# Kernel optimization log

Measured on AMD Instinct MI355X. Metric: run time of the kernel, lower is better.

Reference implementation:

```python
import jax, jax.numpy as jnp
import numpy as np

T, D, N, K, H, F = 2048, 4096, 32, 8, 128, 14336
THETA = 500000.0
EPS = 1e-5


def setup_inputs() -> dict:
    key = jax.random.key(0)
    ks = jax.random.split(key, 10)
    s = 0.02  # weight init scale
    return {
        "x": jax.random.normal(ks[0], (T, D), jnp.float32),
        "positions": jnp.arange(T, dtype=jnp.int32),
        "ln1_scale": jnp.ones((D,), jnp.float32),
        "w_q": jax.random.normal(ks[1], (D, N, H), jnp.float32) * s,
        "w_k": jax.random.normal(ks[2], (D, K, H), jnp.float32) * s,
        "w_v": jax.random.normal(ks[3], (D, K, H), jnp.float32) * s,
        "w_o": jax.random.normal(ks[4], (N, H, D), jnp.float32) * s,
        "ln2_scale": jnp.ones((D,), jnp.float32),
        "w_gate": jax.random.normal(ks[5], (D, F), jnp.float32) * s,
        "w_up": jax.random.normal(ks[6], (D, F), jnp.float32) * s,
        "w_down": jax.random.normal(ks[7], (F, D), jnp.float32) * s,
    }


def _rms_norm(x, scale):
    var = jnp.mean(jnp.square(x), axis=-1, keepdims=True)
    return x * jax.lax.rsqrt(var + EPS) * scale


def _apply_rope(x, pos):
    # x: [T, heads, H]; Llama rotate-half RoPE
    half = H // 2
    inv_freq = 1.0 / (THETA ** (jnp.arange(half, dtype=jnp.float32) / half))
    ang = pos.astype(jnp.float32)[:, None] * inv_freq[None, :]      # [T, half]
    cos = jnp.cos(ang)[:, None, :]
    sin = jnp.sin(ang)[:, None, :]
    x1, x2 = x[..., :half], x[..., half:]
    return jnp.concatenate([x1 * cos - x2 * sin, x2 * cos + x1 * sin], axis=-1)


def reference(x, positions, ln1_scale, w_q, w_k, w_v, w_o, ln2_scale, w_gate, w_up, w_down):
    # --- input RMSNorm ---
    h = _rms_norm(x, ln1_scale)
    # --- QKV projections + RoPE ---
    q = _apply_rope(jnp.einsum('td,dnh->tnh', h, w_q), positions)   # [T,N,H]
    k = _apply_rope(jnp.einsum('td,dkh->tkh', h, w_k), positions)   # [T,K,H]
    v = jnp.einsum('td,dkh->tkh', h, w_v)                            # [T,K,H]
    # --- GQA causal attention (prefill) ---
    G = N // K
    qg = q.reshape(T, K, G, H)
    scale = 1.0 / jnp.sqrt(jnp.float32(H))
    scores = jnp.einsum('tkgh,skh->kgts', qg, k) * scale             # [K,G,T,T]
    causal = positions[:, None] >= positions[None, :]                # [T,T]
    scores = jnp.where(causal[None, None], scores, jnp.finfo(scores.dtype).min)
    probs = jax.nn.softmax(scores, axis=-1)
    attn = jnp.einsum('kgts,skh->tkgh', probs, v).reshape(T, N, H)
    attn_out = jnp.einsum('tnh,nhd->td', attn, w_o)
    # --- residual ---
    residual = attn_out + x
    # --- post-attn RMSNorm + SwiGLU MLP ---
    h2 = _rms_norm(residual, ln2_scale)
    gate = jax.nn.silu(h2 @ w_gate)
    up = h2 @ w_up
    out = (gate * up) @ w_down
    return residual + out
```

## Files before the change

### kernel.cpp

```cpp
#include <hip/hip_runtime.h>

typedef __attribute__((ext_vector_type(8))) short bf16x8;
typedef __attribute__((ext_vector_type(4))) float f32x4;

constexpr int T = 2048;
constexpr int D = 4096;
constexpr int NQ = 32;
constexpr int NKV = 8;
constexpr int H = 128;
constexpr int F = 14336;
constexpr int NQKV = (NQ + 2 * NKV) * H;
constexpr int VOFF = (NQ + NKV) * H;

__device__ inline unsigned short f2bf(float f) {
  unsigned u = __float_as_uint(f);
  return (unsigned short)((u + 0x7FFFu + ((u >> 16) & 1u)) >> 16);
}

__device__ inline void gload_lds16(const void* g, void* l) {
  __builtin_amdgcn_global_load_lds((const __attribute__((address_space(1))) void*)g,
                                   (__attribute__((address_space(3))) void*)l, 16, 0, 0);
}

#define MFMA16(a, b, c) __builtin_amdgcn_mfma_f32_16x16x32_bf16(a, b, c, 0, 0, 0)

template <int MODE>
__global__ __launch_bounds__(256) void transpose_bf16(const float* __restrict__ in,
                                                      unsigned short* __restrict__ out,
                                                      int K, int N) {
  __shared__ float tile[64 * 65];
  const int kb = blockIdx.x * 64;
  const int nb = blockIdx.y * 64;
  const int tid = threadIdx.x;
  const int r = tid >> 2;
  const int c4 = tid & 3;
#pragma unroll
  for (int i = 0; i < 4; ++i) {
    float4 v = *(const float4*)(in + (size_t)(kb + r) * N + nb + c4 * 16 + i * 4);
    *(float4*)&tile[r * 65 + c4 * 16 + i * 4] = v;
  }
  __syncthreads();
  const int n = tid >> 2;
  const int kq = tid & 3;
  int nsrc = nb + n;
  int prow = (MODE == 0) ? nsrc : ((nsrc >> 4) * 32 + (nsrc & 15) + (MODE == 2 ? 16 : 0));
#pragma unroll
  for (int half = 0; half < 2; ++half) {
    ushort4 o0, o1;
    int k0 = kq * 16 + half * 8;
    o0.x = f2bf(tile[(k0 + 0) * 65 + n]);
    o0.y = f2bf(tile[(k0 + 1) * 65 + n]);
    o0.z = f2bf(tile[(k0 + 2) * 65 + n]);
    o0.w = f2bf(tile[(k0 + 3) * 65 + n]);
    o1.x = f2bf(tile[(k0 + 4) * 65 + n]);
    o1.y = f2bf(tile[(k0 + 5) * 65 + n]);
    o1.z = f2bf(tile[(k0 + 6) * 65 + n]);
    o1.w = f2bf(tile[(k0 + 7) * 65 + n]);
    unsigned short* op = out + (size_t)prow * K + kb + k0;
    *(ushort4*)(op + 0) = o0;
    *(ushort4*)(op + 4) = o1;
  }
}

__global__ __launch_bounds__(256) void rmsnorm_kernel(
    const float* __restrict__ in, const float* __restrict__ scale,
    unsigned short* __restrict__ out) {
  int row = blockIdx.x;
  const float4* xr = (const float4*)(in + (size_t)row * D);
  const float4* sr = (const float4*)scale;
  float4 vals[4];
  float ss = 0.f;
#pragma unroll
  for (int i = 0; i < 4; ++i) {
    float4 v = xr[threadIdx.x + i * 256];
    vals[i] = v;
    ss += v.x * v.x + v.y * v.y + v.z * v.z + v.w * v.w;
  }
#pragma unroll
  for (int off = 32; off; off >>= 1) ss += __shfl_xor(ss, off, 64);
  __shared__ float wsum[4];
  if ((threadIdx.x & 63) == 0) wsum[threadIdx.x >> 6] = ss;
  __syncthreads();
  float r = rsqrtf((wsum[0] + wsum[1] + wsum[2] + wsum[3]) * (1.f / D) + 1e-5f);
#pragma unroll
  for (int i = 0; i < 4; ++i) {
    int vi = threadIdx.x + i * 256;
    float4 v = vals[i];
    float4 s = sr[vi];
    ushort4 o;
    o.x = f2bf(v.x * r * s.x);
    o.y = f2bf(v.y * r * s.y);
    o.z = f2bf(v.z * r * s.z);
    o.w = f2bf(v.w * r * s.w);
    *(ushort4*)(out + (size_t)row * D + (size_t)vi * 4) = o;
  }
}

__global__ __launch_bounds__(256) void rmsnorm_add3(
    const float* __restrict__ a, const float* __restrict__ b,
    const float* __restrict__ c, const float* __restrict__ scale,
    float* __restrict__ residOut, unsigned short* __restrict__ out) {
  int row = blockIdx.x;
  const float4* ar = (const float4*)(a + (size_t)row * D);
  const float4* br = (const float4*)(b + (size_t)row * D);
  const float4* cr = (const float4*)(c + (size_t)row * D);
  const float4* sr = (const float4*)scale;
  float4* rr = (float4*)(residOut + (size_t)row * D);
  float4 vals[4];
  float ss = 0.f;
#pragma unroll
  for (int i = 0; i < 4; ++i) {
    int vi = threadIdx.x + i * 256;
    float4 va = ar[vi], vb = br[vi], vc = cr[vi];
    float4 v;
    v.x = va.x + vb.x + vc.x;
    v.y = va.y + vb.y + vc.y;
    v.z = va.z + vb.z + vc.z;
    v.w = va.w + vb.w + vc.w;
    vals[i] = v;
    ss += v.x * v.x + v.y * v.y + v.z * v.z + v.w * v.w;
  }
#pragma unroll
  for (int off = 32; off; off >>= 1) ss += __shfl_xor(ss, off, 64);
  __shared__ float wsum[4];
  if ((threadIdx.x & 63) == 0) wsum[threadIdx.x >> 6] = ss;
  __syncthreads();
  float r = rsqrtf((wsum[0] + wsum[1] + wsum[2] + wsum[3]) * (1.f / D) + 1e-5f);
#pragma unroll
  for (int i = 0; i < 4; ++i) {
    int vi = threadIdx.x + i * 256;
    float4 v = vals[i];
    rr[vi] = v;
    float4 s = sr[vi];
    ushort4 o;
    o.x = f2bf(v.x * r * s.x);
    o.y = f2bf(v.y * r * s.y);
    o.z = f2bf(v.z * r * s.z);
    o.w = f2bf(v.w * r * s.w);
    *(ushort4*)(out + (size_t)row * D + (size_t)vi * 4) = o;
  }
}

__global__ __launch_bounds__(256) void add3_kernel(const float* __restrict__ a,
                                                   const float* __restrict__ b,
                                                   const float* __restrict__ c,
                                                   float* __restrict__ o) {
  int i = blockIdx.x * 256 + threadIdx.x;
  float4 va = ((const float4*)a)[i];
  float4 vb = ((const float4*)b)[i];
  float4 vc = ((const float4*)c)[i];
  float4 vo;
  vo.x = va.x + vb.x + vc.x;
  vo.y = va.y + vb.y + vc.y;
  vo.z = va.z + vb.z + vc.z;
  vo.w = va.w + vb.w + vc.w;
  ((float4*)o)[i] = vo;
}

__global__ __launch_bounds__(256) void rope_table(const int* __restrict__ pos,
                                                  float* __restrict__ ctab,
                                                  float* __restrict__ stab) {
  int idx = blockIdx.x * 256 + threadIdx.x;
  int t = idx >> 6, i = idx & 63;
  float inv = exp2f(-(float)i * (log2f(500000.0f) / 64.0f));
  float ang = (float)pos[t] * inv;
  ctab[idx] = cosf(ang);
  stab[idx] = sinf(ang);
}

__global__ __launch_bounds__(256) void rope_bf16(const float* __restrict__ x,
                                                 const float* __restrict__ ctab,
                                                 const float* __restrict__ stab,
                                                 unsigned short* __restrict__ out,
                                                 int nheads, int row_stride, float scale) {
  int idx = blockIdx.x * 256 + threadIdx.x;
  int i = idx & 63;
  int tn = idx >> 6;
  int t = tn / nheads;
  int n = tn - t * nheads;
  float c = ctab[t * 64 + i], s = stab[t * 64 + i];
  const float* p = x + (size_t)t * row_stride + n * H;
  float x1 = p[i], x2 = p[i + 64];
  unsigned short* o = out + (size_t)tn * H;
  o[i] = f2bf((x1 * c - x2 * s) * scale);
  o[i + 64] = f2bf((x2 * c + x1 * s) * scale);
}

template <int EP>
__global__ __launch_bounds__(512, 1) void gemm256(
    const unsigned short* __restrict__ A, const unsigned short* __restrict__ Bt,
    float* __restrict__ outF, float* __restrict__ outF2,
    unsigned short* __restrict__ outB, int Kd, int Nd, int Klen) {
  __shared__ unsigned short lds[65536];
  const int tid = threadIdx.x, lane = tid & 63, wv = tid >> 6;
  const int wm = wv >> 2, wn = wv & 3;
  const int rl = lane & 15, g = lane >> 4;
  const int kz = blockIdx.z;
  int raw = blockIdx.x + blockIdx.y * gridDim.x;
  int cpx = (gridDim.x * gridDim.y) >> 3;
  int sid = (raw & 7) * cpx + (raw >> 3);
  int brow = sid % gridDim.x;
  int bcol = sid / gridDim.x;
  const int m0 = brow * 256, n0 = bcol * 256;

  const int l8 = lane >> 3;
  const int scol = ((lane & 7) ^ l8) * 8;
  const int xr = (rl & 7) << 4;
  const int pc0 = (g * 16) ^ xr;
  const int pc1 = (64 + g * 16) ^ xr;

  const char* ldsc = (const char*)lds;
  const unsigned short* gA = A + (size_t)(m0 + wv * 8 + l8) * Kd + kz * Klen + scol;
  const unsigned short* gB = Bt + (size_t)(n0 + wv * 8 + l8) * Kd + kz * Klen + scol;

  f32x4 acc[8][4];
#pragma unroll
  for (int i = 0; i < 8; ++i)
#pragma unroll
    for (int j = 0; j < 4; ++j) acc[i][j] = (f32x4){0.f, 0.f, 0.f, 0.f};

  const int NT = Klen >> 6;

#define STAGE_AL(kt, l)                                                      \
  gload_lds16(gA + (size_t)(kt) * 64 + (size_t)(l) * 64 * Kd,                \
              (void*)&lds[((kt) & 1) * 32768 + (l) * 4096 + wv * 512]);
#define STAGE_BL(kt, l)                                                      \
  gload_lds16(gB + (size_t)(kt) * 64 + (size_t)(l) * 64 * Kd,                \
              (void*)&lds[((kt) & 1) * 32768 + 16384 + (l) * 4096 + wv * 512]);
#define SBAR()                        \
  __builtin_amdgcn_sched_barrier(0);  \
  __builtin_amdgcn_s_barrier();

  STAGE_AL(0, 0); STAGE_AL(0, 1); STAGE_AL(0, 2); STAGE_AL(0, 3);
  STAGE_BL(0, 0); STAGE_BL(0, 1); STAGE_BL(0, 2); STAGE_BL(0, 3);
  STAGE_AL(1, 0); STAGE_AL(1, 1); STAGE_AL(1, 2); STAGE_AL(1, 3);
  STAGE_BL(1, 0); STAGE_BL(1, 1); STAGE_BL(1, 2); STAGE_BL(1, 3);
  asm volatile("s_waitcnt vmcnt(8)" ::: "memory");
  SBAR();

  const int bhalf = (wn >> 1) * 16384;
  const int brl = (wn & 1) * 64;

  for (int kt = 0; kt < NT; ++kt) {
    const int b = kt & 1;
    const char* aB = ldsc + b * 65536 + wm * 16384;
    const char* bB = ldsc + b * 65536 + 32768 + bhalf;
    const bool pre = (kt + 2 < NT);
    bf16x8 aR[8][2], bR[4][2];
#pragma unroll
    for (int mf = 0; mf < 8; ++mf) {
      aR[mf][0] = *(const bf16x8*)(aB + (mf * 16 + rl) * 128 + pc0);
      aR[mf][1] = *(const bf16x8*)(aB + (mf * 16 + rl) * 128 + pc1);
    }
#pragma unroll
    for (int nf = 0; nf < 4; ++nf) {
      bR[nf][0] = *(const bf16x8*)(bB + (brl + nf * 16 + rl) * 128 + pc0);
      bR[nf][1] = *(const bf16x8*)(bB + (brl + nf * 16 + rl) * 128 + pc1);
    }
    SBAR();
    if (pre) {
      STAGE_AL(kt + 2, 0); STAGE_AL(kt + 2, 1);
      STAGE_AL(kt + 2, 2); STAGE_AL(kt + 2, 3);
      STAGE_BL(kt + 2, 0); STAGE_BL(kt + 2, 1);
      STAGE_BL(kt + 2, 2); STAGE_BL(kt + 2, 3);
    }
    __builtin_amdgcn_s_setprio(1);
#pragma unroll
    for (int mf = 0; mf < 8; ++mf)
#pragma unroll
      for (int nf = 0; nf < 4; ++nf) {
        acc[mf][nf] = MFMA16(aR[mf][0], bR[nf][0], acc[mf][nf]);
        acc[mf][nf] = MFMA16(aR[mf][1], bR[nf][1], acc[mf][nf]);
      }
    __builtin_amdgcn_s_setprio(0);
    if (pre) {
      asm volatile("s_waitcnt vmcnt(8)" ::: "memory");
    } else if (kt + 1 < NT) {
      asm volatile("s_waitcnt vmcnt(0)" ::: "memory");
    }
    SBAR();
  }

  const int g4 = g * 4;
  if constexpr (EP == 5) {
    const int acolBase = ((n0 + wn * 64) >> 1) + rl;
#pragma unroll
    for (int mf = 0; mf < 8; ++mf)
#pragma unroll
      for (int p = 0; p < 2; ++p) {
        int acol = acolBase + p * 16;
#pragma unroll
        for (int jj = 0; jj < 4; ++jj) {
          int row = m0 + wm * 128 + mf * 16 + g4 + jj;
          float gg = acc[mf][2 * p][jj];
          float uu = acc[mf][2 * p + 1][jj];
          outB[(size_t)row * F + acol] = f2bf(gg / (1.f + __expf(-gg)) * uu);
        }
      }
  } else if constexpr (EP == 4) {
    if (n0 >= VOFF) {
#pragma unroll
      for (int mf = 0; mf < 8; ++mf)
#pragma unroll
        for (int q = 0; q < 4; ++q) {
          int col = n0 + wn * 64 + q * 16 + rl;
          int row0 = m0 + wm * 128 + mf * 16 + g4;
          ushort4 o;
          o.x = f2bf(acc[mf][q][0]);
          o.y = f2bf(acc[mf][q][1]);
          o.z = f2bf(acc[mf][q][2]);
          o.w = f2bf(acc[mf][q][3]);
          *(ushort4*)&outB[(size_t)(col - VOFF) * T + row0] = o;
        }
    } else {
#pragma unroll
      for (int mf = 0; mf < 8; ++mf)
#pragma unroll
        for (int q = 0; q < 4; ++q) {
          int col = n0 + wn * 64 + q * 16 + rl;
#pragma unroll
          for (int jj = 0; jj < 4; ++jj) {
            int row = m0 + wm * 128 + mf * 16 + g4 + jj;
            outF[(size_t)row * Nd + col] = acc[mf][q][jj];
          }
        }
    }
  } else {
    float* dst = kz ? outF2 : outF;
#pragma unroll
    for (int mf = 0; mf < 8; ++mf)
#pragma unroll
      for (int q = 0; q < 4; ++q) {
        int col = n0 + wn * 64 + q * 16 + rl;
#pragma unroll
        for (int jj = 0; jj < 4; ++jj) {
          int row = m0 + wm * 128 + mf * 16 + g4 + jj;
          dst[(size_t)row * Nd + col] = acc[mf][q][jj];
        }
      }
  }
#undef STAGE_AL
#undef STAGE_BL
#undef SBAR
}

constexpr int KLD = 136;
constexpr int VLD = 72;
constexpr int PLD = 72;

__global__ __launch_bounds__(512) void flash_attn(
    const unsigned short* __restrict__ qbf, const unsigned short* __restrict__ kbf,
    const unsigned short* __restrict__ vtbf, unsigned short* __restrict__ out) {
  __shared__ unsigned short K_lds[64 * KLD];
  __shared__ unsigned short Vt_lds[H * VLD];
  __shared__ unsigned short P_lds[8 * 16 * PLD];

  const int tid = threadIdx.x;
  const int lane = tid & 63;
  const int wv = tid >> 6;
  const int qb = blockIdx.x;
  const int kvh = blockIdx.y;
  const int qh = wv & 3, rh = wv >> 2;
  const int n = kvh * 4 + qh;
  const int g = lane >> 4;
  const int rl = lane & 15;
  const int qrow = qb * 32 + rh * 16;

  bf16x8 qfrag[4];
  {
    const unsigned short* qp = qbf + ((size_t)(qrow + rl) * NQ + n) * H + g * 8;
#pragma unroll
    for (int ks = 0; ks < 4; ++ks) qfrag[ks] = *(const bf16x8*)(qp + ks * 32);
  }

  f32x4 oacc[8];
#pragma unroll
  for (int ob = 0; ob < 8; ++ob) oacc[ob] = (f32x4){0.f, 0.f, 0.f, 0.f};
  float mrun[4] = {-1e30f, -1e30f, -1e30f, -1e30f};
  float lrun[4] = {0.f, 0.f, 0.f, 0.f};

  const int krow = tid >> 3, kseg = (tid & 7) * 16;
  const int vh = tid >> 2, vseg = (tid & 3) * 16;

  const int ktmax = (qb * 32 + 31) >> 6;
  bf16x8 krA, krB, vrA, vrB;
  {
    const unsigned short* kp = kbf + ((size_t)krow * NKV + kvh) * H + kseg;
    krA = *(const bf16x8*)kp;
    krB = *(const bf16x8*)(kp + 8);
    const unsigned short* vp = vtbf + (size_t)(kvh * H + vh) * T + vseg;
    vrA = *(const bf16x8*)vp;
    vrB = *(const bf16x8*)(vp + 8);
  }
  for (int kt = 0; kt <= ktmax; ++kt) {
    const int kbase = kt * 64;
    __syncthreads();
    *(bf16x8*)&K_lds[krow * KLD + kseg] = krA;
    *(bf16x8*)&K_lds[krow * KLD + kseg + 8] = krB;
    *(bf16x8*)&Vt_lds[vh * VLD + vseg] = vrA;
    *(bf16x8*)&Vt_lds[vh * VLD + vseg + 8] = vrB;
    if (kt < ktmax) {
      const unsigned short* kp =
          kbf + ((size_t)(kbase + 64 + krow) * NKV + kvh) * H + kseg;
      krA = *(const bf16x8*)kp;
      krB = *(const bf16x8*)(kp + 8);
      const unsigned short* vp =
          vtbf + (size_t)(kvh * H + vh) * T + kbase + 64 + vseg;
      vrA = *(const bf16x8*)vp;
      vrB = *(const bf16x8*)(vp + 8);
    }
    __syncthreads();

    f32x4 sacc[4];
#pragma unroll
    for (int cb = 0; cb < 4; ++cb) sacc[cb] = (f32x4){0.f, 0.f, 0.f, 0.f};
#pragma unroll
    for (int cb = 0; cb < 4; ++cb)
#pragma unroll
      for (int ks = 0; ks < 4; ++ks) {
        bf16x8 kf = *(const bf16x8*)&K_lds[(cb * 16 + rl) * KLD + ks * 32 + g * 8];
        sacc[cb] = MFMA16(qfrag[ks], kf, sacc[cb]);
      }

    if (kt == ktmax) {
#pragma unroll
      for (int cb = 0; cb < 4; ++cb) {
        int kv_abs = kbase + cb * 16 + rl;
#pragma unroll
        for (int r = 0; r < 4; ++r) {
          if (kv_abs > qrow + g * 4 + r) sacc[cb][r] = -1e30f;
        }
      }
    }

    float mx[4], sm[4], corr[4];
#pragma unroll
    for (int r = 0; r < 4; ++r) {
      float m0 = fmaxf(fmaxf(sacc[0][r], sacc[1][r]), fmaxf(sacc[2][r], sacc[3][r]));
#pragma unroll
      for (int off = 1; off < 16; off <<= 1) m0 = fmaxf(m0, __shfl_xor(m0, off, 64));
      float nm = fmaxf(mrun[r], m0);
      corr[r] = __expf(mrun[r] - nm);
      mrun[r] = nm;
      mx[r] = nm;
    }
#pragma unroll
    for (int cb = 0; cb < 4; ++cb)
#pragma unroll
      for (int r = 0; r < 4; ++r) sacc[cb][r] = __expf(sacc[cb][r] - mx[r]);
#pragma unroll
    for (int r = 0; r < 4; ++r) {
      float s0 = sacc[0][r] + sacc[1][r] + sacc[2][r] + sacc[3][r];
#pragma unroll
      for (int off = 1; off < 16; off <<= 1) s0 += __shfl_xor(s0, off, 64);
      sm[r] = s0;
      lrun[r] = lrun[r] * corr[r] + sm[r];
    }
#pragma unroll
    for (int ob = 0; ob < 8; ++ob)
#pragma unroll
      for (int r = 0; r < 4; ++r) oacc[ob][r] *= corr[r];

#pragma unroll
    for (int cb = 0; cb < 4; ++cb)
#pragma unroll
      for (int r = 0; r < 4; ++r)
        P_lds[(wv * 16 + g * 4 + r) * PLD + cb * 16 + rl] = f2bf(sacc[cb][r]);

    bf16x8 pa[2];
#pragma unroll
    for (int ks = 0; ks < 2; ++ks)
      pa[ks] = *(const bf16x8*)&P_lds[(wv * 16 + rl) * PLD + ks * 32 + g * 8];

#pragma unroll
    for (int ob = 0; ob < 8; ++ob)
#pragma unroll
      for (int ks = 0; ks < 2; ++ks) {
        bf16x8 vf = *(const bf16x8*)&Vt_lds[(ob * 16 + rl) * VLD + ks * 32 + g * 8];
        oacc[ob] = MFMA16(pa[ks], vf, oacc[ob]);
      }
  }

  float inv[4];
#pragma unroll
  for (int r = 0; r < 4; ++r) inv[r] = 1.f / lrun[r];
#pragma unroll
  for (int ob = 0; ob < 8; ++ob)
#pragma unroll
    for (int r = 0; r < 4; ++r) {
      int t = qrow + g * 4 + r;
      out[((size_t)t * NQ + n) * H + ob * 16 + rl] = f2bf(oacc[ob][r] * inv[r]);
    }
}

extern "C" void kernel_launch(void* const* d_in, const int* in_sizes, int n_in,
                              void* d_out, int out_size, void* d_ws, size_t ws_size,
                              hipStream_t stream) {
  (void)in_sizes; (void)n_in; (void)out_size; (void)ws_size;
  const float* x = (const float*)d_in[0];
  const int* positions = (const int*)d_in[1];
  const float* ln1 = (const float*)d_in[2];
  const float* w_q = (const float*)d_in[3];
  const float* w_k = (const float*)d_in[4];
  const float* w_v = (const float*)d_in[5];
  const float* w_o = (const float*)d_in[6];
  const float* ln2 = (const float*)d_in[7];
  const float* w_gate = (const float*)d_in[8];
  const float* w_up = (const float*)d_in[9];
  const float* w_down = (const float*)d_in[10];
  float* out = (float*)d_out;

  char* ws = (char*)d_ws;
  size_t off = 0;
  auto alloc = [&](size_t bytes) {
    char* p = ws + off;
    off += (bytes + 255) & ~(size_t)255;
    return p;
  };
  unsigned short* h_bf = (unsigned short*)alloc((size_t)T * D * 2);
  unsigned short* h2_bf = (unsigned short*)alloc((size_t)T * D * 2);
  unsigned short* attn_bf = (unsigned short*)alloc((size_t)T * NQ * H * 2);
  unsigned short* act_bf = (unsigned short*)alloc((size_t)T * F * 2);
  float* qkvf = (float*)alloc((size_t)T * NQKV * 4);
  float* resid = (float*)alloc((size_t)T * D * 4);
  float* ctab = (float*)alloc((size_t)T * 64 * 4);
  float* stab = (float*)alloc((size_t)T * 64 * 4);
  unsigned short* qbf = (unsigned short*)alloc((size_t)T * NQ * H * 2);
  unsigned short* kbf = (unsigned short*)alloc((size_t)T * NKV * H * 2);
  unsigned short* vtbf = (unsigned short*)alloc((size_t)NKV * H * T * 2);
  unsigned short* wqkvt = (unsigned short*)alloc((size_t)NQKV * D * 2);
  unsigned short* wot = (unsigned short*)alloc((size_t)D * NQ * H * 2);
  unsigned short* wgut = (unsigned short*)alloc((size_t)2 * F * D * 2);
  unsigned short* wdt = (unsigned short*)alloc((size_t)D * F * 2);
  float* part0 = qkvf;
  float* part1 = (float*)wqkvt;

  transpose_bf16<0><<<dim3(D / 64, (NQ * H) / 64), 256, 0, stream>>>(w_q, wqkvt, D, NQ * H);
  transpose_bf16<0><<<dim3(D / 64, (NKV * H) / 64), 256, 0, stream>>>(
      w_k, wqkvt + (size_t)NQ * H * D, D, NKV * H);
  transpose_bf16<0><<<dim3(D / 64, (NKV * H) / 64), 256, 0, stream>>>(
      w_v, wqkvt + (size_t)VOFF * D, D, NKV * H);
  transpose_bf16<0><<<dim3((NQ * H) / 64, D / 64), 256, 0, stream>>>(w_o, wot, NQ * H, D);
  transpose_bf16<1><<<dim3(D / 64, F / 64), 256, 0, stream>>>(w_gate, wgut, D, F);
  transpose_bf16<2><<<dim3(D / 64, F / 64), 256, 0, stream>>>(w_up, wgut, D, F);
  transpose_bf16<0><<<dim3(F / 64, D / 64), 256, 0, stream>>>(w_down, wdt, F, D);

  rmsnorm_kernel<<<T, 256, 0, stream>>>(x, ln1, h_bf);
  rope_table<<<(T * 64) / 256, 256, 0, stream>>>(positions, ctab, stab);
  gemm256<4><<<dim3(T / 256, NQKV / 256, 1), 512, 0, stream>>>(
      h_bf, wqkvt, qkvf, nullptr, vtbf, D, NQKV, D);
  rope_bf16<<<(T * NQ * 64) / 256, 256, 0, stream>>>(qkvf, ctab, stab, qbf, NQ, NQKV,
                                                     0.08838834764831845f);
  rope_bf16<<<(T * NKV * 64) / 256, 256, 0, stream>>>(qkvf + NQ * H, ctab, stab, kbf,
                                                      NKV, NQKV, 1.0f);
  flash_attn<<<dim3(T / 32, NKV), 512, 0, stream>>>(qbf, kbf, vtbf, attn_bf);
  gemm256<0><<<dim3(T / 256, D / 256, 2), 512, 0, stream>>>(
      attn_bf, wot, part0, part1, nullptr, NQ * H, D, NQ * H / 2);
  rmsnorm_add3<<<T, 256, 0, stream>>>(part0, part1, x, ln2, resid, h2_bf);
  gemm256<5><<<dim3(T / 256, (2 * F) / 256), 512, 0, stream>>>(
      h2_bf, wgut, nullptr, nullptr, act_bf, D, 2 * F, D);
  gemm256<0><<<dim3(T / 256, D / 256, 2), 512, 0, stream>>>(
      act_bf, wdt, part0, part1, nullptr, F, D, F / 2);
  add3_kernel<<<(T * D / 4) / 256, 256, 0, stream>>>(part0, part1, resid, out);
}
```

Before: 1.331 ms.

## Split GEMM k-tile into quadrant phases, interleave LDS reads and prefetch; bf16 QK output

Restructures the 256x256 GEMM main loop into four MFMA quadrant phases, with LDS fragment reads and global-to-LDS prefetches spread between them. The low B fragments for the next tile are carried across iterations in registers. The goal is to overlap LDS reads and memory issue with MFMA work instead of loading every fragment up front. The launch bound changes to request two blocks per CU, which limits register use and could cause spills given the 128 accumulator floats. Separately, the QKV GEMM now writes Q and K as bf16 instead of fp32, and the RoPE kernel reads that bf16 input, halving that intermediate traffic at the cost of rounding before RoPE.

```diff
diff --git a/kernel.cpp b/kernel.cpp
--- a/kernel.cpp
+++ b/kernel.cpp
@@ -15,6 +15,10 @@
 __device__ inline unsigned short f2bf(float f) {
   unsigned u = __float_as_uint(f);
   return (unsigned short)((u + 0x7FFFu + ((u >> 16) & 1u)) >> 16);
+}
+
+__device__ inline float bf2f(unsigned short u) {
+  return __uint_as_float((unsigned)u << 16);
 }
 
 __device__ inline void gload_lds16(const void* g, void* l) {
@@ -168,7 +172,7 @@
   stab[idx] = sinf(ang);
 }
 
-__global__ __launch_bounds__(256) void rope_bf16(const float* __restrict__ x,
+__global__ __launch_bounds__(256) void rope_bf16(const unsigned short* __restrict__ x,
                                                  const float* __restrict__ ctab,
                                                  const float* __restrict__ stab,
                                                  unsigned short* __restrict__ out,
@@ -179,15 +183,15 @@
   int t = tn / nheads;
   int n = tn - t * nheads;
   float c = ctab[t * 64 + i], s = stab[t * 64 + i];
-  const float* p = x + (size_t)t * row_stride + n * H;
-  float x1 = p[i], x2 = p[i + 64];
+  const unsigned short* p = x + (size_t)t * row_stride + n * H;
+  float x1 = bf2f(p[i]), x2 = bf2f(p[i + 64]);
   unsigned short* o = out + (size_t)tn * H;
   o[i] = f2bf((x1 * c - x2 * s) * scale);
   o[i + 64] = f2bf((x2 * c + x1 * s) * scale);
 }
 
 template <int EP>
-__global__ __launch_bounds__(512, 1) void gemm256(
+__global__ __launch_bounds__(512, 2) void gemm256(
     const unsigned short* __restrict__ A, const unsigned short* __restrict__ Bt,
     float* __restrict__ outF, float* __restrict__ outF2,
     unsigned short* __restrict__ outB, int Kd, int Nd, int Klen) {
@@ -221,64 +225,113 @@
 
   const int NT = Klen >> 6;
 
-#define STAGE_AL(kt, l)                                                      \
+#define STAGE_AL(kt, bb, l)                                                  \
   gload_lds16(gA + (size_t)(kt) * 64 + (size_t)(l) * 64 * Kd,                \
-              (void*)&lds[((kt) & 1) * 32768 + (l) * 4096 + wv * 512]);
-#define STAGE_BL(kt, l)                                                      \
+              (void*)&lds[(bb) * 32768 + (l) * 4096 + wv * 512]);
+#define STAGE_BL(kt, bb, l)                                                  \
   gload_lds16(gB + (size_t)(kt) * 64 + (size_t)(l) * 64 * Kd,                \
-              (void*)&lds[((kt) & 1) * 32768 + 16384 + (l) * 4096 + wv * 512]);
+              (void*)&lds[(bb) * 32768 + 16384 + (l) * 4096 + wv * 512]);
 #define SBAR()                        \
   __builtin_amdgcn_sched_barrier(0);  \
   __builtin_amdgcn_s_barrier();
 
-  STAGE_AL(0, 0); STAGE_AL(0, 1); STAGE_AL(0, 2); STAGE_AL(0, 3);
-  STAGE_BL(0, 0); STAGE_BL(0, 1); STAGE_BL(0, 2); STAGE_BL(0, 3);
-  STAGE_AL(1, 0); STAGE_AL(1, 1); STAGE_AL(1, 2); STAGE_AL(1, 3);
-  STAGE_BL(1, 0); STAGE_BL(1, 1); STAGE_BL(1, 2); STAGE_BL(1, 3);
+  STAGE_AL(0, 0, 0); STAGE_AL(0, 0, 1); STAGE_AL(0, 0, 2); STAGE_AL(0, 0, 3);
+  STAGE_BL(0, 0, 0); STAGE_BL(0, 0, 1); STAGE_BL(0, 0, 2); STAGE_BL(0, 0, 3);
+  STAGE_AL(1, 1, 0); STAGE_AL(1, 1, 1); STAGE_AL(1, 1, 2); STAGE_AL(1, 1, 3);
+  STAGE_BL(1, 1, 0); STAGE_BL(1, 1, 1); STAGE_BL(1, 1, 2); STAGE_BL(1, 1, 3);
   asm volatile("s_waitcnt vmcnt(8)" ::: "memory");
   SBAR();
 
   const int bhalf = (wn >> 1) * 16384;
   const int brl = (wn & 1) * 64;
 
-  for (int kt = 0; kt < NT; ++kt) {
-    const int b = kt & 1;
-    const char* aB = ldsc + b * 65536 + wm * 16384;
-    const char* bB = ldsc + b * 65536 + 32768 + bhalf;
-    const bool pre = (kt + 2 < NT);
-    bf16x8 aR[8][2], bR[4][2];
-#pragma unroll
-    for (int mf = 0; mf < 8; ++mf) {
-      aR[mf][0] = *(const bf16x8*)(aB + (mf * 16 + rl) * 128 + pc0);
-      aR[mf][1] = *(const bf16x8*)(aB + (mf * 16 + rl) * 128 + pc1);
+  bf16x8 bLoC[2][2];
+  {
+    const char* bB0 = ldsc + 32768 + bhalf;
+#pragma unroll
+    for (int nf = 0; nf < 2; ++nf) {
+      bLoC[nf][0] = *(const bf16x8*)(bB0 + (brl + nf * 16 + rl) * 128 + pc0);
+      bLoC[nf][1] = *(const bf16x8*)(bB0 + (brl + nf * 16 + rl) * 128 + pc1);
     }
-#pragma unroll
-    for (int nf = 0; nf < 4; ++nf) {
-      bR[nf][0] = *(const bf16x8*)(bB + (brl + nf * 16 + rl) * 128 + pc0);
-      bR[nf][1] = *(const bf16x8*)(bB + (brl + nf * 16 + rl) * 128 + pc1);
-    }
-    SBAR();
-    if (pre) {
-      STAGE_AL(kt + 2, 0); STAGE_AL(kt + 2, 1);
-      STAGE_AL(kt + 2, 2); STAGE_AL(kt + 2, 3);
-      STAGE_BL(kt + 2, 0); STAGE_BL(kt + 2, 1);
-      STAGE_BL(kt + 2, 2); STAGE_BL(kt + 2, 3);
-    }
-    __builtin_amdgcn_s_setprio(1);
-#pragma unroll
-    for (int mf = 0; mf < 8; ++mf)
-#pragma unroll
-      for (int nf = 0; nf < 4; ++nf) {
-        acc[mf][nf] = MFMA16(aR[mf][0], bR[nf][0], acc[mf][nf]);
-        acc[mf][nf] = MFMA16(aR[mf][1], bR[nf][1], acc[mf][nf]);
-      }
-    __builtin_amdgcn_s_setprio(0);
-    if (pre) {
-      asm volatile("s_waitcnt vmcnt(8)" ::: "memory");
-    } else if (kt + 1 < NT) {
-      asm volatile("s_waitcnt vmcnt(0)" ::: "memory");
-    }
-    SBAR();
+  }
+
+#define KTILE(kt, bb)                                                          \
+  {                                                                            \
+    const char* aB = ldsc + (bb) * 65536 + wm * 16384;                         \
+    const char* bB = ldsc + (bb) * 65536 + 32768 + bhalf;                      \
+    const char* bBn = ldsc + (1 - (bb)) * 65536 + 32768 + bhalf;               \
+    const bool pre = ((kt) + 2 < NT);                                          \
+    bf16x8 aLo[4][2], aHi[4][2], bHi[2][2], bLoN[2][2];                        \
+    _Pragma("unroll") for (int mf = 0; mf < 4; ++mf) {                         \
+      aLo[mf][0] = *(const bf16x8*)(aB + (mf * 16 + rl) * 128 + pc0);          \
+      aLo[mf][1] = *(const bf16x8*)(aB + (mf * 16 + rl) * 128 + pc1);          \
+    }                                                                          \
+    SBAR();                                                                    \
+    __builtin_amdgcn_s_setprio(1);                                             \
+    _Pragma("unroll") for (int mf = 0; mf < 4; ++mf)                           \
+        _Pragma("unroll") for (int nf = 0; nf < 2; ++nf) {                     \
+      acc[mf][nf] = MFMA16(aLo[mf][0], bLoC[nf][0], acc[mf][nf]);              \
+      acc[mf][nf] = MFMA16(aLo[mf][1], bLoC[nf][1], acc[mf][nf]);              \
+    }                                                                          \
+    __builtin_amdgcn_s_setprio(0);                                             \
+    _Pragma("unroll") for (int nf = 0; nf < 2; ++nf) {                         \
+      bHi[nf][0] = *(const bf16x8*)(bB + (brl + (nf + 2) * 16 + rl) * 128 + pc0); \
+      bHi[nf][1] = *(const bf16x8*)(bB + (brl + (nf + 2) * 16 + rl) * 128 + pc1); \
+    }                                                                          \
+    if (pre) { STAGE_AL((kt) + 2, bb, 0); STAGE_AL((kt) + 2, bb, 2); }         \
+    SBAR();                                                                    \
+    __builtin_amdgcn_s_setprio(1);                                             \
+    _Pragma("unroll") for (int mf = 0; mf < 4; ++mf)                           \
+        _Pragma("unroll") for (int nf = 0; nf < 2; ++nf) {                     \
+      acc[mf][nf + 2] = MFMA16(aLo[mf][0], bHi[nf][0], acc[mf][nf + 2]);       \
+      acc[mf][nf + 2] = MFMA16(aLo[mf][1], bHi[nf][1], acc[mf][nf + 2]);       \
+    }                                                                          \
+    __builtin_amdgcn_s_setprio(0);                                             \
+    _Pragma("unroll") for (int mf = 0; mf < 4; ++mf) {                         \
+      aHi[mf][0] = *(const bf16x8*)(aB + ((mf + 4) * 16 + rl) * 128 + pc0);    \
+      aHi[mf][1] = *(const bf16x8*)(aB + ((mf + 4) * 16 + rl) * 128 + pc1);    \
+    }                                                                          \
+    if (pre) {                                                                 \
+      STAGE_BL((kt) + 2, bb, 0); STAGE_BL((kt) + 2, bb, 1);                    \
+      STAGE_BL((kt) + 2, bb, 2); STAGE_BL((kt) + 2, bb, 3);                    \
+      asm volatile("s_waitcnt vmcnt(6)" ::: "memory");                         \
+    } else {                                                                   \
+      asm volatile("s_waitcnt vmcnt(0)" ::: "memory");                         \
+    }                                                                          \
+    SBAR();                                                                    \
+    __builtin_amdgcn_s_setprio(1);                                             \
+    _Pragma("unroll") for (int mf = 0; mf < 4; ++mf)                           \
+        _Pragma("unroll") for (int nf = 0; nf < 2; ++nf) {                     \
+      acc[mf + 4][nf + 2] = MFMA16(aHi[mf][0], bHi[nf][0], acc[mf + 4][nf + 2]); \
+      acc[mf + 4][nf + 2] = MFMA16(aHi[mf][1], bHi[nf][1], acc[mf + 4][nf + 2]); \
+    }                                                                          \
+    __builtin_amdgcn_s_setprio(0);                                             \
+    if (pre) { STAGE_AL((kt) + 2, bb, 1); STAGE_AL((kt) + 2, bb, 3); }         \
+    if ((kt) + 1 < NT) {                                                       \
+      _Pragma("unroll") for (int nf = 0; nf < 2; ++nf) {                       \
+        bLoN[nf][0] = *(const bf16x8*)(bBn + (brl + nf * 16 + rl) * 128 + pc0); \
+        bLoN[nf][1] = *(const bf16x8*)(bBn + (brl + nf * 16 + rl) * 128 + pc1); \
+      }                                                                        \
+    }                                                                          \
+    SBAR();                                                                    \
+    __builtin_amdgcn_s_setprio(1);                                             \
+    _Pragma("unroll") for (int mf = 0; mf < 4; ++mf)                           \
+        _Pragma("unroll") for (int nf = 0; nf < 2; ++nf) {                     \
+      acc[mf + 4][nf] = MFMA16(aHi[mf][0], bLoC[nf][0], acc[mf + 4][nf]);      \
+      acc[mf + 4][nf] = MFMA16(aHi[mf][1], bLoC[nf][1], acc[mf + 4][nf]);      \
+    }                                                                          \
+    __builtin_amdgcn_s_setprio(0);                                             \
+    if ((kt) + 1 < NT) {                                                       \
+      _Pragma("unroll") for (int nf = 0; nf < 2; ++nf) {                       \
+        bLoC[nf][0] = bLoN[nf][0];                                             \
+        bLoC[nf][1] = bLoN[nf][1];                                             \
+      }                                                                        \
+    }                                                                          \
+  }
+
+  for (int kt2 = 0; kt2 < NT; kt2 += 2) {
+    KTILE(kt2, 0);
+    KTILE(kt2 + 1, 1);
   }
 
   const int g4 = g * 4;
@@ -313,6 +366,7 @@
           *(ushort4*)&outB[(size_t)(col - VOFF) * T + row0] = o;
         }
     } else {
+      unsigned short* qk = (unsigned short*)outF;
 #pragma unroll
       for (int mf = 0; mf < 8; ++mf)
 #pragma unroll
@@ -321,7 +375,7 @@
 #pragma unroll
           for (int jj = 0; jj < 4; ++jj) {
             int row = m0 + wm * 128 + mf * 16 + g4 + jj;
-            outF[(size_t)row * Nd + col] = acc[mf][q][jj];
+            qk[(size_t)row * VOFF + col] = f2bf(acc[mf][q][jj]);
           }
         }
     }
@@ -339,6 +393,7 @@
         }
       }
   }
+#undef KTILE
 #undef STAGE_AL
 #undef STAGE_BL
 #undef SBAR
@@ -534,6 +589,7 @@
   unsigned short* wdt = (unsigned short*)alloc((size_t)D * F * 2);
   float* part0 = qkvf;
   float* part1 = (float*)wqkvt;
+  unsigned short* qkbf = (unsigned short*)qkvf;
 
   transpose_bf16<0><<<dim3(D / 64, (NQ * H) / 64), 256, 0, stream>>>(w_q, wqkvt, D, NQ * H);
   transpose_bf16<0><<<dim3(D / 64, (NKV * H) / 64), 256, 0, stream>>>(
@@ -549,10 +605,10 @@
   rope_table<<<(T * 64) / 256, 256, 0, stream>>>(positions, ctab, stab);
   gemm256<4><<<dim3(T / 256, NQKV / 256, 1), 512, 0, stream>>>(
       h_bf, wqkvt, qkvf, nullptr, vtbf, D, NQKV, D);
-  rope_bf16<<<(T * NQ * 64) / 256, 256, 0, stream>>>(qkvf, ctab, stab, qbf, NQ, NQKV,
+  rope_bf16<<<(T * NQ * 64) / 256, 256, 0, stream>>>(qkbf, ctab, stab, qbf, NQ, VOFF,
                                                      0.08838834764831845f);
-  rope_bf16<<<(T * NKV * 64) / 256, 256, 0, stream>>>(qkvf + NQ * H, ctab, stab, kbf,
-                                                      NKV, NQKV, 1.0f);
+  rope_bf16<<<(T * NKV * 64) / 256, 256, 0, stream>>>(qkbf + NQ * H, ctab, stab, kbf,
+                                                      NKV, VOFF, 1.0f);
   flash_attn<<<dim3(T / 32, NKV), 512, 0, stream>>>(qbf, kbf, vtbf, attn_bf);
   gemm256<0><<<dim3(T / 256, D / 256, 2), 512, 0, stream>>>(
       attn_bf, wot, part0, part1, nullptr, NQ * H, D, NQ * H / 2);
```

After: 1.354 ms. No clear change (+1.7%).
